# Optimization experiments

Measured on AMD Instinct MI355X. Metric: run time of the kernel, lower is better.

The kernel has to match this reference:

```python
import jax, jax.numpy as jnp
import numpy as np

IN_F = 4096
OUT_F = 4096
M_PAD = 4096   # next pow2 >= OUT_F
N_PAD = 4096   # next pow2 >= IN_F
CB_SIZE = 256  # E8 codebook entries, each an 8-dim vector


def fht(x):
    """Normalized fast Hadamard transform along the last axis (power-of-2 length)."""
    n = x.shape[-1]
    lead = x.shape[:-1]
    x = x.reshape(-1, n)
    h = 1
    while h < n:  # log2(n) static iterations -> jit-friendly
        x = x.reshape(-1, n // (2 * h), 2, h)
        a, b = x[:, :, 0, :], x[:, :, 1, :]
        x = jnp.stack((a + b, a - b), axis=2).reshape(-1, n)
        h *= 2
    return (x * np.float32(1.0 / np.sqrt(n))).reshape(*lead, n)


def setup_inputs() -> dict:
    key = jax.random.key(0)
    k_x, k_q, k_su, k_sv, k_cb = jax.random.split(key, 5)
    x = jax.random.normal(k_x, (4, 2048, IN_F), dtype=jnp.float32)
    Qidxs = jax.random.randint(k_q, (M_PAD, N_PAD // 8), 0, CB_SIZE, dtype=jnp.int32)
    # sign vectors are +-1 (random Hadamard transform signs)
    SU = jnp.where(jax.random.normal(k_su, (M_PAD,)) >= 0, 1.0, -1.0).astype(jnp.float32)
    SV = jnp.where(jax.random.normal(k_sv, (N_PAD,)) >= 0, 1.0, -1.0).astype(jnp.float32)
    Wscale = jnp.ones((), dtype=jnp.float32)
    codebook = jax.random.normal(k_cb, (CB_SIZE, 8), dtype=jnp.float32)
    return {"x": x, "Qidxs": Qidxs, "SU": SU, "SV": SV, "Wscale": Wscale, "codebook": codebook}


def reference(x, Qidxs, SU, SV, Wscale, codebook):
    shape = x.shape
    xf = x.reshape(-1, IN_F).astype(jnp.float32)          # (B, in)
    x_pad = jnp.pad(xf, ((0, 0), (0, N_PAD - IN_F)))      # (B, n_pad)
    # 1) input -> RHT domain: sign flip then Hadamard
    x_rht = fht(x_pad * SV[None, :])
    # 2) decode codebook indices into dense RHT-domain weight (m_pad, n_pad)
    W_rht = codebook[Qidxs.reshape(-1)].reshape(M_PAD, N_PAD)
    # 3) GEMM in RHT domain with global scale
    y_rht = (x_rht @ W_rht.T) * Wscale
    # 4) output RHT inverse: Hadamard then sign flip, unpad
    y = fht(y_rht) * SU[None, :]
    y = y[:, :OUT_F]
    return y.reshape(*shape[:-1], OUT_F)
```

## Files before the change

### kernel.cpp

```cpp
#include <hip/hip_runtime.h>
#include <hip/hip_bf16.h>


using short8 = __attribute__((ext_vector_type(8))) short;
using f32x4  = __attribute__((ext_vector_type(4))) float;

#define AS1 __attribute__((address_space(1)))
#define AS3 __attribute__((address_space(3)))

__device__ __forceinline__ unsigned short f2bf(float f) {
  unsigned int u = __float_as_uint(f);
  unsigned int r = (u + 0x7fffu + ((u >> 16) & 1u)) >> 16;
  return (unsigned short)r;
}

__device__ __forceinline__ void gload16(const void* g, void* l) {
  __builtin_amdgcn_global_load_lds((const AS1 void*)g, (AS3 void*)l, 16, 0, 0);
}

#define WAIT_VM6 asm volatile("s_waitcnt vmcnt(6)" ::: "memory")
#define WAIT_VM4 asm volatile("s_waitcnt vmcnt(4)" ::: "memory")
#define WAIT_VM0 asm volatile("s_waitcnt vmcnt(0)" ::: "memory")

__global__ __launch_bounds__(256) void rht_in_kernel(const float* __restrict__ X,
                                                     const float* __restrict__ SV,
                                                     unsigned short* __restrict__ A) {
  __shared__ float tmp[4096];
  const int row = blockIdx.x;
  const int t = threadIdx.x;
  const size_t base = (size_t)row * 4096;
  float v[16];
#pragma unroll
  for (int j = 0; j < 16; ++j) {
    int c = j * 256 + t;
    v[j] = X[base + c] * SV[c];
  }
#pragma unroll
  for (int d = 1; d < 16; d <<= 1) {
#pragma unroll
    for (int j = 0; j < 16; ++j) {
      if ((j & d) == 0) {
        float a = v[j], b = v[j | d];
        v[j] = a + b;
        v[j | d] = a - b;
      }
    }
  }
  const int lane = t & 63;
#pragma unroll
  for (int d = 1; d < 64; d <<= 1) {
#pragma unroll
    for (int j = 0; j < 16; ++j) {
      float p = __shfl_xor(v[j], d, 64);
      v[j] = (lane & d) ? (p - v[j]) : (v[j] + p);
    }
  }
#pragma unroll
  for (int dd = 0; dd < 2; ++dd) {
    const int d = 64 << dd;
    if (dd) __syncthreads();
#pragma unroll
    for (int j = 0; j < 16; ++j) tmp[j * 256 + t] = v[j];
    __syncthreads();
#pragma unroll
    for (int j = 0; j < 16; ++j) {
      float p = tmp[j * 256 + (t ^ d)];
      v[j] = (t & d) ? (p - v[j]) : (v[j] + p);
    }
  }
#pragma unroll
  for (int j = 0; j < 16; ++j) A[base + j * 256 + t] = f2bf(v[j]);
}

__global__ __launch_bounds__(256) void decode_w_kernel(const int* __restrict__ Q,
                                                       const float* __restrict__ cb,
                                                       unsigned short* __restrict__ W) {
  const int e = blockIdx.x * 256 + threadIdx.x;
  const int idx = Q[e];
  const float4* c = (const float4*)(cb + (size_t)idx * 8);
  float4 c0 = c[0], c1 = c[1];
  union { short8 v; unsigned short u[8]; } w;
  w.u[0] = f2bf(c0.x); w.u[1] = f2bf(c0.y); w.u[2] = f2bf(c0.z); w.u[3] = f2bf(c0.w);
  w.u[4] = f2bf(c1.x); w.u[5] = f2bf(c1.y); w.u[6] = f2bf(c1.z); w.u[7] = f2bf(c1.w);
  *(short8*)&W[(size_t)e * 8] = w.v;
}

#define MFMA1(mi, ni, av, bv) \
  acc[mi][ni] = __builtin_amdgcn_mfma_f32_16x16x32_bf16(av, bv, acc[mi][ni], 0, 0, 0)

#define STAGE_A(BB, H, KTN) do {                                          \
  const unsigned short* gp_ = Ag + (KTN) * 64 + (H) * 32;                 \
  gload16(gp_, (unsigned short*)&sA[BB][H][0][0] + d0);                   \
  gload16(gp_ + (size_t)128 * 4096, (unsigned short*)&sA[BB][H][0][0] + d1); \
} while (0)

#define STAGE_B(BB, H, KTN) do {                                          \
  const unsigned short* gp_ = Bg + (KTN) * 64 + (H) * 32;                 \
  gload16(gp_, (unsigned short*)&sB[BB][H][0][0] + d0);                   \
  gload16(gp_ + (size_t)128 * 4096, (unsigned short*)&sB[BB][H][0][0] + d1); \
} while (0)

#define PH(BC, KS, MB, RDB, STG, WT) do {                                 \
  short8 a0_ = *(const short8*)&sA[BC][KS][wm + (MB + 0) * 16 + fr][qc];  \
  short8 a1_ = *(const short8*)&sA[BC][KS][wm + (MB + 1) * 16 + fr][qc];  \
  short8 a2_ = *(const short8*)&sA[BC][KS][wm + (MB + 2) * 16 + fr][qc];  \
  short8 a3_ = *(const short8*)&sA[BC][KS][wm + (MB + 3) * 16 + fr][qc];  \
  if (RDB) {                                                              \
    bf0 = *(const short8*)&sB[BC][KS][wn + 0 * 16 + fr][qc];              \
    bf1 = *(const short8*)&sB[BC][KS][wn + 1 * 16 + fr][qc];              \
    bf2 = *(const short8*)&sB[BC][KS][wn + 2 * 16 + fr][qc];              \
    bf3 = *(const short8*)&sB[BC][KS][wn + 3 * 16 + fr][qc];              \
  }                                                                       \
  STG;                                                                    \
  __builtin_amdgcn_s_barrier();                                           \
  asm volatile("s_waitcnt lgkmcnt(0)" ::: "memory");                      \
  __builtin_amdgcn_s_setprio(1);                                          \
  MFMA1(MB + 0, 0, a0_, bf0); MFMA1(MB + 0, 1, a0_, bf1);                 \
  MFMA1(MB + 0, 2, a0_, bf2); MFMA1(MB + 0, 3, a0_, bf3);                 \
  MFMA1(MB + 1, 0, a1_, bf0); MFMA1(MB + 1, 1, a1_, bf1);                 \
  MFMA1(MB + 1, 2, a1_, bf2); MFMA1(MB + 1, 3, a1_, bf3);                 \
  MFMA1(MB + 2, 0, a2_, bf0); MFMA1(MB + 2, 1, a2_, bf1);                 \
  MFMA1(MB + 2, 2, a2_, bf2); MFMA1(MB + 2, 3, a2_, bf3);                 \
  MFMA1(MB + 3, 0, a3_, bf0); MFMA1(MB + 3, 1, a3_, bf1);                 \
  MFMA1(MB + 3, 2, a3_, bf2); MFMA1(MB + 3, 3, a3_, bf3);                 \
  __builtin_amdgcn_s_setprio(0);                                          \
  WT;                                                                     \
  __builtin_amdgcn_s_barrier();                                           \
} while (0)

#define TILE(BC, BN_, KTN, DS, LASTF) do {                                \
  PH(BC, 0, 0, 1,                                                         \
     { if (DS) { STAGE_A(BN_, 0, KTN); STAGE_B(BN_, 0, KTN); } }, {});    \
  PH(BC, 0, 4, 0, { if (DS) { STAGE_A(BN_, 1, KTN); } },                  \
     { if (LASTF) { WAIT_VM0; } else { WAIT_VM6; } });                    \
  PH(BC, 1, 0, 1, { if (DS) { STAGE_B(BN_, 1, KTN); } }, {});             \
  PH(BC, 1, 4, 0, {}, { if (!(LASTF)) { WAIT_VM4; } });                   \
} while (0)

__global__ __launch_bounds__(512, 2) void gemm_bt_kernel(const unsigned short* __restrict__ A,
                                                         const unsigned short* __restrict__ B,
                                                         float* __restrict__ C) {
  __shared__ unsigned short sA[2][2][256][32];
  __shared__ unsigned short sB[2][2][256][32];

  const int bid = blockIdx.x;
  const int swz = (bid & 7) * 64 + (bid >> 3);
  const int tm = swz >> 4;
  const int tn = swz & 15;

  const int t = threadIdx.x;
  const int lane = t & 63;
  const int w = t >> 6;
  const int wm = (w >> 2) * 128;
  const int wn = (w & 3) * 64;
  const int fr = lane & 15;
  const int qc = ((lane >> 4) ^ ((lane >> 1) & 3)) * 8;

  const int sr = t >> 2;
  const int sc = ((t & 3) ^ ((t >> 3) & 3)) * 8;
  const unsigned short* Ag = A + (size_t)(tm * 256 + sr) * 4096 + sc;
  const unsigned short* Bg = B + (size_t)(tn * 256 + sr) * 4096 + sc;
  const int d0 = t * 8;
  const int d1 = (512 + t) * 8;

  f32x4 acc[8][4];
#pragma unroll
  for (int m = 0; m < 8; ++m)
#pragma unroll
    for (int n = 0; n < 4; ++n) {
      f32x4 z = {0.f, 0.f, 0.f, 0.f};
      acc[m][n] = z;
    }
  short8 bf0, bf1, bf2, bf3;

  STAGE_A(0, 0, 0); STAGE_B(0, 0, 0); STAGE_A(0, 1, 0); STAGE_B(0, 1, 0);
  WAIT_VM4;
  __builtin_amdgcn_s_barrier();

  for (int k2 = 0; k2 < 31; ++k2) {
    TILE(0, 1, 2 * k2 + 1, 1, 0);
    TILE(1, 0, 2 * k2 + 2, 1, 0);
  }
  TILE(0, 1, 63, 1, 0);
  TILE(1, 0, 64, 0, 1);

  const size_t crow0 = (size_t)tm * 256 + wm + (lane >> 4) * 4;
  const int ccol0 = tn * 256 + wn + fr;
#pragma unroll
  for (int mf = 0; mf < 8; ++mf)
#pragma unroll
    for (int j = 0; j < 4; ++j) {
      float* Cp = C + (crow0 + mf * 16 + j) * 4096 + ccol0;
#pragma unroll
      for (int nf = 0; nf < 4; ++nf)
        __builtin_nontemporal_store(acc[mf][nf][j], Cp + nf * 16);
    }
}

__global__ __launch_bounds__(256) void rht_out_kernel(float* __restrict__ Y,
                                                      const float* __restrict__ SU,
                                                      const float* __restrict__ Wscale) {
  __shared__ float tmp[4096];
  const int row = blockIdx.x;
  const int t = threadIdx.x;
  const size_t base = (size_t)row * 4096;
  float v[16];
#pragma unroll
  for (int j = 0; j < 16; ++j) v[j] = Y[base + j * 256 + t];
#pragma unroll
  for (int d = 1; d < 16; d <<= 1) {
#pragma unroll
    for (int j = 0; j < 16; ++j) {
      if ((j & d) == 0) {
        float a = v[j], b = v[j | d];
        v[j] = a + b;
        v[j | d] = a - b;
      }
    }
  }
  const int lane = t & 63;
#pragma unroll
  for (int d = 1; d < 64; d <<= 1) {
#pragma unroll
    for (int j = 0; j < 16; ++j) {
      float p = __shfl_xor(v[j], d, 64);
      v[j] = (lane & d) ? (p - v[j]) : (v[j] + p);
    }
  }
#pragma unroll
  for (int dd = 0; dd < 2; ++dd) {
    const int d = 64 << dd;
    if (dd) __syncthreads();
#pragma unroll
    for (int j = 0; j < 16; ++j) tmp[j * 256 + t] = v[j];
    __syncthreads();
#pragma unroll
    for (int j = 0; j < 16; ++j) {
      float p = tmp[j * 256 + (t ^ d)];
      v[j] = (t & d) ? (p - v[j]) : (v[j] + p);
    }
  }
  const float ws = Wscale[0] * (1.0f / 4096.0f);
#pragma unroll
  for (int j = 0; j < 16; ++j) {
    int c = j * 256 + t;
    __builtin_nontemporal_store(v[j] * SU[c] * ws, &Y[base + c]);
  }
}

extern "C" void kernel_launch(void* const* d_in, const int* in_sizes, int n_in,
                              void* d_out, int out_size, void* d_ws, size_t ws_size,
                              hipStream_t stream) {
  const float* x      = (const float*)d_in[0];
  const int*   Qidxs  = (const int*)d_in[1];
  const float* SU     = (const float*)d_in[2];
  const float* SV     = (const float*)d_in[3];
  const float* Wscale = (const float*)d_in[4];
  const float* cb     = (const float*)d_in[5];
  float* out = (float*)d_out;

  unsigned short* Arht = (unsigned short*)d_ws;
  unsigned short* W    = (unsigned short*)((char*)d_ws + (size_t)8192 * 4096 * 2);

  rht_in_kernel<<<8192, 256, 0, stream>>>(x, SV, Arht);
  decode_w_kernel<<<(4096 * 512) / 256, 256, 0, stream>>>(Qidxs, cb, W);
  gemm_bt_kernel<<<512, 512, 0, stream>>>(Arht, W, out);
  rht_out_kernel<<<8192, 256, 0, stream>>>(out, SU, Wscale);
}
```

Measured before the change: 385.2 us.

## Software-pipeline LDS fragment reads one phase ahead of MFMAs in GEMM tile

The GEMM inner tile is restructured so the A/B fragment reads for the next phase are issued from LDS before the current phase's 16 MFMAs run, using double register sets. Sched barriers pin the ordering, and global-to-LDS staging is interleaved with the vmcnt waits adjusted. The goal is to hide LDS read latency behind MFMA execution, at the cost of more VGPRs at two waves per SIMD. Nontemporal stores in the GEMM epilogue and the output RHT are also replaced with regular stores, which changes how the output writes interact with cache.

```diff
diff --git a/kernel.cpp b/kernel.cpp
--- a/kernel.cpp
+++ b/kernel.cpp
@@ -18,9 +18,13 @@
   __builtin_amdgcn_global_load_lds((const AS1 void*)g, (AS3 void*)l, 16, 0, 0);
 }
 
-#define WAIT_VM6 asm volatile("s_waitcnt vmcnt(6)" ::: "memory")
 #define WAIT_VM4 asm volatile("s_waitcnt vmcnt(4)" ::: "memory")
 #define WAIT_VM0 asm volatile("s_waitcnt vmcnt(0)" ::: "memory")
+#define LGKM0    asm volatile("s_waitcnt lgkmcnt(0)" ::: "memory")
+#define SB       __builtin_amdgcn_sched_barrier(0)
+#define BAR      __builtin_amdgcn_s_barrier()
+#define PRIO1    __builtin_amdgcn_s_setprio(1)
+#define PRIO0    __builtin_amdgcn_s_setprio(0)
 
 __global__ __launch_bounds__(256) void rht_in_kernel(const float* __restrict__ X,
                                                      const float* __restrict__ SV,
@@ -88,6 +92,31 @@
 #define MFMA1(mi, ni, av, bv) \
   acc[mi][ni] = __builtin_amdgcn_mfma_f32_16x16x32_bf16(av, bv, acc[mi][ni], 0, 0, 0)
 
+#define MFMA16(MB, a0_, a1_, a2_, a3_, bx0, bx1, bx2, bx3) do {           \
+  MFMA1(MB + 0, 0, a0_, bx0); MFMA1(MB + 0, 1, a0_, bx1);                 \
+  MFMA1(MB + 0, 2, a0_, bx2); MFMA1(MB + 0, 3, a0_, bx3);                 \
+  MFMA1(MB + 1, 0, a1_, bx0); MFMA1(MB + 1, 1, a1_, bx1);                 \
+  MFMA1(MB + 1, 2, a1_, bx2); MFMA1(MB + 1, 3, a1_, bx3);                 \
+  MFMA1(MB + 2, 0, a2_, bx0); MFMA1(MB + 2, 1, a2_, bx1);                 \
+  MFMA1(MB + 2, 2, a2_, bx2); MFMA1(MB + 2, 3, a2_, bx3);                 \
+  MFMA1(MB + 3, 0, a3_, bx0); MFMA1(MB + 3, 1, a3_, bx1);                 \
+  MFMA1(MB + 3, 2, a3_, bx2); MFMA1(MB + 3, 3, a3_, bx3);                 \
+} while (0)
+
+#define RD_A4(r0, r1, r2, r3, BC, KS, MB) do {                            \
+  r0 = *(const short8*)&sA[BC][KS][wm + (MB + 0) * 16 + fr][qc];          \
+  r1 = *(const short8*)&sA[BC][KS][wm + (MB + 1) * 16 + fr][qc];          \
+  r2 = *(const short8*)&sA[BC][KS][wm + (MB + 2) * 16 + fr][qc];          \
+  r3 = *(const short8*)&sA[BC][KS][wm + (MB + 3) * 16 + fr][qc];          \
+} while (0)
+
+#define RD_B4(r0, r1, r2, r3, BC, KS) do {                                \
+  r0 = *(const short8*)&sB[BC][KS][wn + 0 * 16 + fr][qc];                 \
+  r1 = *(const short8*)&sB[BC][KS][wn + 1 * 16 + fr][qc];                 \
+  r2 = *(const short8*)&sB[BC][KS][wn + 2 * 16 + fr][qc];                 \
+  r3 = *(const short8*)&sB[BC][KS][wn + 3 * 16 + fr][qc];                 \
+} while (0)
+
 #define STAGE_A(BB, H, KTN) do {                                          \
   const unsigned short* gp_ = Ag + (KTN) * 64 + (H) * 32;                 \
   gload16(gp_, (unsigned short*)&sA[BB][H][0][0] + d0);                   \
@@ -100,41 +129,36 @@
   gload16(gp_ + (size_t)128 * 4096, (unsigned short*)&sB[BB][H][0][0] + d1); \
 } while (0)
 
-#define PH(BC, KS, MB, RDB, STG, WT) do {                                 \
-  short8 a0_ = *(const short8*)&sA[BC][KS][wm + (MB + 0) * 16 + fr][qc];  \
-  short8 a1_ = *(const short8*)&sA[BC][KS][wm + (MB + 1) * 16 + fr][qc];  \
-  short8 a2_ = *(const short8*)&sA[BC][KS][wm + (MB + 2) * 16 + fr][qc];  \
-  short8 a3_ = *(const short8*)&sA[BC][KS][wm + (MB + 3) * 16 + fr][qc];  \
-  if (RDB) {                                                              \
-    bf0 = *(const short8*)&sB[BC][KS][wn + 0 * 16 + fr][qc];              \
-    bf1 = *(const short8*)&sB[BC][KS][wn + 1 * 16 + fr][qc];              \
-    bf2 = *(const short8*)&sB[BC][KS][wn + 2 * 16 + fr][qc];              \
-    bf3 = *(const short8*)&sB[BC][KS][wn + 3 * 16 + fr][qc];              \
-  }                                                                       \
-  STG;                                                                    \
-  __builtin_amdgcn_s_barrier();                                           \
-  asm volatile("s_waitcnt lgkmcnt(0)" ::: "memory");                      \
-  __builtin_amdgcn_s_setprio(1);                                          \
-  MFMA1(MB + 0, 0, a0_, bf0); MFMA1(MB + 0, 1, a0_, bf1);                 \
-  MFMA1(MB + 0, 2, a0_, bf2); MFMA1(MB + 0, 3, a0_, bf3);                 \
-  MFMA1(MB + 1, 0, a1_, bf0); MFMA1(MB + 1, 1, a1_, bf1);                 \
-  MFMA1(MB + 1, 2, a1_, bf2); MFMA1(MB + 1, 3, a1_, bf3);                 \
-  MFMA1(MB + 2, 0, a2_, bf0); MFMA1(MB + 2, 1, a2_, bf1);                 \
-  MFMA1(MB + 2, 2, a2_, bf2); MFMA1(MB + 2, 3, a2_, bf3);                 \
-  MFMA1(MB + 3, 0, a3_, bf0); MFMA1(MB + 3, 1, a3_, bf1);                 \
-  MFMA1(MB + 3, 2, a3_, bf2); MFMA1(MB + 3, 3, a3_, bf3);                 \
-  __builtin_amdgcn_s_setprio(0);                                          \
-  WT;                                                                     \
-  __builtin_amdgcn_s_barrier();                                           \
-} while (0)
-
 #define TILE(BC, BN_, KTN, DS, LASTF) do {                                \
-  PH(BC, 0, 0, 1,                                                         \
-     { if (DS) { STAGE_A(BN_, 0, KTN); STAGE_B(BN_, 0, KTN); } }, {});    \
-  PH(BC, 0, 4, 0, { if (DS) { STAGE_A(BN_, 1, KTN); } },                  \
-     { if (LASTF) { WAIT_VM0; } else { WAIT_VM6; } });                    \
-  PH(BC, 1, 0, 1, { if (DS) { STAGE_B(BN_, 1, KTN); } }, {});             \
-  PH(BC, 1, 4, 0, {}, { if (!(LASTF)) { WAIT_VM4; } });                   \
+           \
+  RD_A4(aS0_0, aS0_1, aS0_2, aS0_3, BC, 0, 0);                            \
+  RD_B4(bA_0, bA_1, bA_2, bA_3, BC, 0);                                   \
+  if (DS) { STAGE_A(BN_, 0, KTN); }                                       \
+  BAR; LGKM0; SB;                                                         \
+  RD_A4(aS1_0, aS1_1, aS1_2, aS1_3, BC, 0, 4); SB;                        \
+  PRIO1; MFMA16(0, aS0_0, aS0_1, aS0_2, aS0_3, bA_0, bA_1, bA_2, bA_3);   \
+  PRIO0; BAR;                                                             \
+                 \
+  if (DS) { STAGE_B(BN_, 0, KTN); }                                       \
+  BAR; LGKM0; SB;                                                         \
+  if (LASTF) { WAIT_VM0; } else { WAIT_VM4; }                             \
+  RD_A4(aS0_0, aS0_1, aS0_2, aS0_3, BC, 1, 0);                            \
+  RD_B4(bB_0, bB_1, bB_2, bB_3, BC, 1); SB;                               \
+  PRIO1; MFMA16(4, aS1_0, aS1_1, aS1_2, aS1_3, bA_0, bA_1, bA_2, bA_3);   \
+  PRIO0; BAR;                                                             \
+                                     \
+  if (DS) { STAGE_A(BN_, 1, KTN); }                                       \
+  BAR; LGKM0; SB;                                                         \
+  RD_A4(aS1_0, aS1_1, aS1_2, aS1_3, BC, 1, 4); SB;                        \
+  PRIO1; MFMA16(0, aS0_0, aS0_1, aS0_2, aS0_3, bB_0, bB_1, bB_2, bB_3);   \
+  PRIO0; BAR;                                                             \
+            \
+  if (DS) { STAGE_B(BN_, 1, KTN); }                                       \
+  BAR; LGKM0; SB;                                                         \
+  PRIO1; MFMA16(4, aS1_0, aS1_1, aS1_2, aS1_3, bB_0, bB_1, bB_2, bB_3);   \
+  PRIO0;                                                                  \
+  if (!(LASTF)) { WAIT_VM4; }                                             \
+  BAR;                                                                    \
 } while (0)
 
 __global__ __launch_bounds__(512, 2) void gemm_bt_kernel(const unsigned short* __restrict__ A,
@@ -171,11 +195,14 @@
       f32x4 z = {0.f, 0.f, 0.f, 0.f};
       acc[m][n] = z;
     }
-  short8 bf0, bf1, bf2, bf3;
+  short8 aS0_0, aS0_1, aS0_2, aS0_3;
+  short8 aS1_0, aS1_1, aS1_2, aS1_3;
+  short8 bA_0, bA_1, bA_2, bA_3;
+  short8 bB_0, bB_1, bB_2, bB_3;
 
   STAGE_A(0, 0, 0); STAGE_B(0, 0, 0); STAGE_A(0, 1, 0); STAGE_B(0, 1, 0);
   WAIT_VM4;
-  __builtin_amdgcn_s_barrier();
+  BAR;
 
   for (int k2 = 0; k2 < 31; ++k2) {
     TILE(0, 1, 2 * k2 + 1, 1, 0);
@@ -192,8 +219,7 @@
     for (int j = 0; j < 4; ++j) {
       float* Cp = C + (crow0 + mf * 16 + j) * 4096 + ccol0;
 #pragma unroll
-      for (int nf = 0; nf < 4; ++nf)
-        __builtin_nontemporal_store(acc[mf][nf][j], Cp + nf * 16);
+      for (int nf = 0; nf < 4; ++nf) Cp[nf * 16] = acc[mf][nf][j];
     }
 }
 
@@ -244,7 +270,7 @@
 #pragma unroll
   for (int j = 0; j < 16; ++j) {
     int c = j * 256 + t;
-    __builtin_nontemporal_store(v[j] * SU[c] * ws, &Y[base + c]);
+    Y[base + c] = v[j] * SU[c] * ws;
   }
 }
 
```

Measured after the change: 356.3 us. 7.5% less time.
